# Performance work log

Measured on AMD Instinct MI355X. Metric: run time of the kernel, lower is better.

The kernel has to match this reference:

```python
import jax, jax.numpy as jnp
import numpy as np

N = 50000      # nodes
E = 600000     # edges
DIN = 128      # input_dim
H = 128        # hidden_dim
NH = 8         # heads
HD = H // NH   # head_dim = 16
OUT = 128      # output_dim
P = 20000      # pos/neg pair count
EPS = 1e-5


def setup_inputs() -> dict:
    key = jax.random.key(0)
    ks = jax.random.split(key, 20)
    s = 0.05
    inp = {
        "x": jax.random.normal(ks[0], (N, DIN), jnp.float32),
        "edge_index": jax.random.randint(ks[1], (2, E), 0, N),
        "drug_pos_ids": jax.random.randint(ks[2], (P,), 0, N),
        "target_pos_ids": jax.random.randint(ks[3], (P,), 0, N),
        "drug_neg_ids": jax.random.randint(ks[4], (P,), 0, N),
        "target_neg_ids": jax.random.randint(ks[5], (P,), 0, N),
        "adjacency_matrix": jnp.zeros((1,), jnp.float32),  # unused by forward
        # GCN weights stored [in, out]; biases [out]
        "gcn_w0": jax.random.normal(ks[6], (DIN, H), jnp.float32) * s,
        "gcn_b0": jnp.zeros((H,), jnp.float32),
        "gcn_w1": jax.random.normal(ks[7], (H, H), jnp.float32) * s,
        "gcn_b1": jnp.zeros((H,), jnp.float32),
        "gcn_w2": jax.random.normal(ks[8], (H, H), jnp.float32) * s,
        "gcn_b2": jnp.zeros((H,), jnp.float32),
        "wq": jax.random.normal(ks[9], (H, H), jnp.float32) * s,
        "wk": jax.random.normal(ks[10], (H, H), jnp.float32) * s,
        "wv": jax.random.normal(ks[11], (H, H), jnp.float32) * s,
        "ln_g": jnp.ones((H,), jnp.float32),   # shared LayerNorm (same instance reused)
        "ln_b": jnp.zeros((H,), jnp.float32),
        "out_w": jax.random.normal(ks[12], (H, OUT), jnp.float32) * s,
        "out_b": jnp.zeros((OUT,), jnp.float32),
    }
    return inp


def _layernorm(t, g, b):
    mu = t.mean(-1, keepdims=True)
    var = ((t - mu) ** 2).mean(-1, keepdims=True)
    return (t - mu) * jax.lax.rsqrt(var + EPS) * g + b


def reference(x, edge_index, drug_pos_ids, target_pos_ids, drug_neg_ids, target_neg_ids,
              adjacency_matrix, gcn_w0, gcn_b0, gcn_w1, gcn_b1, gcn_w2, gcn_b2,
              wq, wk, wv, ln_g, ln_b, out_w, out_b):
    num_nodes = x.shape[0]
    loop = jnp.arange(num_nodes)
    src = jnp.concatenate([edge_index[0], loop])  # add self-loops (PyG GCNConv default)
    dst = jnp.concatenate([edge_index[1], loop])
    deg = jax.ops.segment_sum(jnp.ones_like(dst, dtype=x.dtype), dst, num_segments=num_nodes)
    dinv = jnp.where(deg > 0, jax.lax.rsqrt(deg), 0.0)
    norm = dinv[src] * dinv[dst]  # [E+N]

    def gcn(h, W, b):
        hw = h @ W                                    # [N,H]
        msg = hw[src] * norm[:, None]                 # gather + scale  [E+N,H]
        return jax.ops.segment_sum(msg, dst, num_segments=num_nodes) + b

    cur = x
    embs = []
    for W, b in ((gcn_w0, gcn_b0), (gcn_w1, gcn_b1), (gcn_w2, gcn_b2)):
        new = jnp.maximum(gcn(cur, W, b), 0.0)
        new = _layernorm(new, ln_g, ln_b)
        # dropout is identity in eval mode
        cur = cur + new if cur.shape == new.shape else new
        embs.append(cur)
    emb = jnp.stack(embs, axis=0)  # [L,N,H]
    L = emb.shape[0]

    def split_heads(t):  # [L,N,H] -> [NH,N,L,HD]
        return t.reshape(L, num_nodes, NH, HD).transpose(2, 1, 0, 3)

    q = split_heads(emb @ wq)
    k = split_heads(emb @ wk)
    v = split_heads(emb @ wv)
    scores = jnp.einsum('hnld,hnmd->hnlm', q, k) / jnp.sqrt(jnp.float32(HD))
    attn = jax.nn.softmax(scores, axis=-1)  # dropout = identity in eval
    ctx = jnp.einsum('hnlm,hnmd->hnld', attn, v)          # [NH,N,L,HD]
    ctx = ctx.transpose(2, 1, 0, 3).reshape(L, num_nodes, H)

    z = _layernorm(ctx, ln_g, ln_b)
    z_last = z[-1] @ out_w + out_b  # [N,OUT]; z_D == z_T in original code
    return (z_last[drug_pos_ids], z_last[target_pos_ids],
            z_last[drug_neg_ids], z_last[target_neg_ids])
```

## Files before the change

kernel.cpp:

```cpp
#include <hip/hip_runtime.h>
#include <math.h>

using bf16x8 = __attribute__((ext_vector_type(8))) short;
using f32x4  = __attribute__((ext_vector_type(4))) float;

__device__ __forceinline__ unsigned short f2b(float f) {
  unsigned u = __float_as_uint(f);
  u += 0x7FFFu + ((u >> 16) & 1u);
  return (unsigned short)(u >> 16);
}
__device__ __forceinline__ float b2f(unsigned short h) {
  return __uint_as_float((unsigned)h << 16);
}
__device__ __forceinline__ float2 upk(unsigned u) {
  return make_float2(__uint_as_float(u << 16), __uint_as_float(u & 0xFFFF0000u));
}


__global__ void k_degree(const int* __restrict__ dst, int* __restrict__ degi, int E) {
  int e = blockIdx.x * blockDim.x + threadIdx.x;
  if (e < E) atomicAdd(&degi[dst[e]], 1);
}

__global__ void k_dinv(const int* __restrict__ degi, float* __restrict__ dinv, int n) {
  int i = blockIdx.x * blockDim.x + threadIdx.x;
  if (i < n) dinv[i] = rsqrtf((float)(degi[i] + 1));
}

__global__ __launch_bounds__(256)
void k_part(const int* __restrict__ deg, int* __restrict__ part, int n) {
  __shared__ int l[256];
  int tid = threadIdx.x, i = blockIdx.x * 256 + tid;
  l[tid] = (i < n) ? deg[i] : 0;
  __syncthreads();
  for (int s = 128; s; s >>= 1) { if (tid < s) l[tid] += l[tid + s]; __syncthreads(); }
  if (!tid) part[blockIdx.x] = l[0];
}

__global__ __launch_bounds__(1024)
void k_scanpart(int* __restrict__ part, int np, int* __restrict__ off_n) {
  __shared__ int l[1024];
  int tid = threadIdx.x;
  int v = (tid < np) ? part[tid] : 0;
  l[tid] = v;
  __syncthreads();
  for (int s = 1; s < 1024; s <<= 1) {
    int t = (tid >= s) ? l[tid - s] : 0;
    __syncthreads();
    l[tid] += t;
    __syncthreads();
  }
  if (tid < np) part[tid] = l[tid] - v;
  if (tid == np - 1) *off_n = l[tid];
}

__global__ __launch_bounds__(256)
void k_off(const int* __restrict__ deg, const int* __restrict__ part,
           int* __restrict__ off, int n) {
  __shared__ int l[256];
  int tid = threadIdx.x, i = blockIdx.x * 256 + tid;
  int v = (i < n) ? deg[i] : 0;
  l[tid] = v;
  __syncthreads();
  for (int s = 1; s < 256; s <<= 1) {
    int t = (tid >= s) ? l[tid - s] : 0;
    __syncthreads();
    l[tid] += t;
    __syncthreads();
  }
  if (i < n) off[i] = part[blockIdx.x] + l[tid] - v;
}

__global__ void k_scatter(const int* __restrict__ srcv, const int* __restrict__ dstv,
                          const float* __restrict__ dinv, const int* __restrict__ off,
                          int* __restrict__ cursor, int* __restrict__ csr_src,
                          float* __restrict__ csr_norm, int E) {
  int e = blockIdx.x * blockDim.x + threadIdx.x;
  if (e >= E) return;
  int d = dstv[e];
  int p = atomicAdd(&cursor[d], 1);
  int slot = off[d] + p;
  int s = srcv[e];
  csr_src[slot] = s;
  csr_norm[slot] = dinv[s] * dinv[d];
}


__global__ void k_cvtx(const float* __restrict__ x, unsigned short* __restrict__ xb,
                       long n4) {
  long t = (long)blockIdx.x * blockDim.x + threadIdx.x;
  if (t >= n4) return;
  float4 v = ((const float4*)x)[t];
  unsigned lo = (unsigned)f2b(v.x) | ((unsigned)f2b(v.y) << 16);
  unsigned hi = (unsigned)f2b(v.z) | ((unsigned)f2b(v.w) << 16);
  ((uint2*)xb)[t] = make_uint2(lo, hi);
}


__global__ __launch_bounds__(256)
void k_cvtw(const float* gw0, const float* gw1, const float* gw2,
            const float* wk, const float* wv, const float* wq, const float* ow,
            unsigned short* gwT0, unsigned short* gwT1, unsigned short* gwT2,
            unsigned short* wkvT, unsigned short* wqT, unsigned short* owT) {
  const float* src; unsigned short* dst;
  switch (blockIdx.y) {
    case 0: src = gw0; dst = gwT0; break;
    case 1: src = gw1; dst = gwT1; break;
    case 2: src = gw2; dst = gwT2; break;
    case 3: src = wk;  dst = wkvT; break;
    case 4: src = wv;  dst = wkvT + 128 * 128; break;
    case 5: src = wq;  dst = wqT; break;
    default: src = ow; dst = owT; break;
  }
  int t = blockIdx.x * 256 + threadIdx.x;
  int r = t >> 7, c = t & 127;
  dst[(long)c * 128 + r] = f2b(src[t]);
}


__global__ __launch_bounds__(128, 6)
void k_gcn_layer(const unsigned short* __restrict__ embp,
                 const int* __restrict__ off, const int* __restrict__ csr_src,
                 const float* __restrict__ csr_norm, const float* __restrict__ dinv,
                 const unsigned short* __restrict__ wT,
                 const float* __restrict__ bias,
                 const float* __restrict__ ln_g, const float* __restrict__ ln_b,
                 unsigned short* __restrict__ embo, int N) {
  __shared__ unsigned a_sw[16 * 64];
  __shared__ float lnsum[16][2], lnsq[16][2];

  int tid = threadIdx.x, lane = tid & 63, w = tid >> 6;
  int g = lane >> 4, c16 = lane & 15;
  long n0 = (long)blockIdx.x * 16;

  for (int t = 0; t < 8; ++t) {
    int row = w * 8 + t;
    long node = n0 + row;
    long nc = node < N ? node : N - 1;
    float dn = dinv[nc];
    int s0 = off[nc], s1 = off[nc + 1];
    float acc[8];
    {
      uint4 rs_ = *(const uint4*)&embp[nc * 128 + c16 * 8];
      float wgt = (g == 0) ? dn * dn : 0.f;
      float2 f;
      f = upk(rs_.x); acc[0] = f.x * wgt; acc[1] = f.y * wgt;
      f = upk(rs_.y); acc[2] = f.x * wgt; acc[3] = f.y * wgt;
      f = upk(rs_.z); acc[4] = f.x * wgt; acc[5] = f.y * wgt;
      f = upk(rs_.w); acc[6] = f.x * wgt; acc[7] = f.y * wgt;
    }
    for (int i = s0; i < s1; i += 16) {
      int id[4]; float nm[4];
#pragma unroll
      for (int u = 0; u < 4; ++u) {
        int j = i + u * 4 + g;
        int jj = j < s1 ? j : s1 - 1;
        id[u] = csr_src[jj];
        nm[u] = j < s1 ? csr_norm[jj] : 0.f;
      }
      uint4 rv[4];
#pragma unroll
      for (int u = 0; u < 4; ++u)
        rv[u] = *(const uint4*)&embp[(long)id[u] * 128 + c16 * 8];
#pragma unroll
      for (int u = 0; u < 4; ++u) {
        float2 f0 = upk(rv[u].x), f1 = upk(rv[u].y);
        float2 f2 = upk(rv[u].z), f3 = upk(rv[u].w);
        acc[0] += f0.x * nm[u]; acc[1] += f0.y * nm[u];
        acc[2] += f1.x * nm[u]; acc[3] += f1.y * nm[u];
        acc[4] += f2.x * nm[u]; acc[5] += f2.y * nm[u];
        acc[6] += f3.x * nm[u]; acc[7] += f3.y * nm[u];
      }
    }
#pragma unroll
    for (int k = 0; k < 8; ++k) {
      acc[k] += __shfl_xor(acc[k], 16);
      acc[k] += __shfl_xor(acc[k], 32);
    }
    if (g == 0) {
      unsigned* dst = (unsigned*)((char*)a_sw +
                      (row * 256 + ((c16 * 16) ^ ((row & 7) << 4))));
      dst[0] = (unsigned)f2b(acc[0]) | ((unsigned)f2b(acc[1]) << 16);
      dst[1] = (unsigned)f2b(acc[2]) | ((unsigned)f2b(acc[3]) << 16);
      dst[2] = (unsigned)f2b(acc[4]) | ((unsigned)f2b(acc[5]) << 16);
      dst[3] = (unsigned)f2b(acc[6]) | ((unsigned)f2b(acc[7]) << 16);
    }
  }
  __syncthreads();

  int lo = lane & 15, hi = lane >> 4;
  int cb0 = w * 64;
  f32x4 acc2[4] = {};
#pragma unroll
  for (int ks = 0; ks < 4; ++ks) {
    int k0 = ks * 32 + hi * 8;
    bf16x8 a = *(const bf16x8*)((char*)a_sw + lo * 256 + ((k0 * 2) ^ ((lo & 7) << 4)));
#pragma unroll
    for (int cf = 0; cf < 4; ++cf) {
      bf16x8 b = *(const bf16x8*)&wT[(long)(cb0 + cf * 16 + lo) * 128 + k0];
      acc2[cf] = __builtin_amdgcn_mfma_f32_16x16x32_bf16(a, b, acc2[cf], 0, 0, 0);
    }
  }

  float vreg[4][4];
#pragma unroll
  for (int j = 0; j < 4; ++j) {
    float s = 0.f, q = 0.f;
#pragma unroll
    for (int cf = 0; cf < 4; ++cf) {
      int col = cb0 + cf * 16 + lo;
      float v = fmaxf(acc2[cf][j] + bias[col], 0.f);
      vreg[cf][j] = v;
      s += v; q += v * v;
    }
#pragma unroll
    for (int m = 1; m < 16; m <<= 1) { s += __shfl_xor(s, m); q += __shfl_xor(q, m); }
    if (lo == 0) { lnsum[hi * 4 + j][w] = s; lnsq[hi * 4 + j][w] = q; }
  }
  __syncthreads();
#pragma unroll
  for (int j = 0; j < 4; ++j) {
    int row = hi * 4 + j;
    float sum = lnsum[row][0] + lnsum[row][1];
    float sq  = lnsq[row][0] + lnsq[row][1];
    float mu = sum * (1.f / 128.f);
    float var = sq * (1.f / 128.f) - mu * mu;
    float rs = rsqrtf(var + 1e-5f);
    long gr = n0 + row;
    if (gr < N) {
#pragma unroll
      for (int cf = 0; cf < 4; ++cf) {
        int col = cb0 + cf * 16 + lo;
        float z = (vreg[cf][j] - mu) * rs * ln_g[col] + ln_b[col]
                  + b2f(embp[gr * 128 + col]);
        embo[gr * 128 + col] = f2b(z);
      }
    }
  }
}


__global__ __launch_bounds__(256)
void k_attn_fused(const unsigned short* __restrict__ emb,
                  const unsigned short* __restrict__ wkvT,
                  const unsigned short* __restrict__ wqT,
                  const unsigned short* __restrict__ owT,
                  const float* __restrict__ ln_g, const float* __restrict__ ln_b,
                  const float* __restrict__ out_b,
                  unsigned short* __restrict__ zoutb, int N) {
  __shared__ unsigned short kvl[48 * 256];
  __shared__ unsigned short ql[16 * 128];
  __shared__ unsigned short zl[16 * 128];

  int tid = threadIdx.x, lane = tid & 63, w = tid >> 6;
  int lo = lane & 15, hi = lane >> 4;
  long n0 = (long)blockIdx.x * 16;
  long nr = n0 + lo; if (nr >= N) nr = N - 1;

  {
    int cb0 = w * 64;
    f32x4 acc[3][4] = {};
#pragma unroll
    for (int ks = 0; ks < 4; ++ks) {
      int k0 = ks * 32 + hi * 8;
      bf16x8 a[3];
#pragma unroll
      for (int l = 0; l < 3; ++l)
        a[l] = *(const bf16x8*)&emb[((long)l * N + nr) * 128 + k0];
#pragma unroll
      for (int cf = 0; cf < 4; ++cf) {
        bf16x8 b = *(const bf16x8*)&wkvT[(long)(cb0 + cf * 16 + lo) * 128 + k0];
#pragma unroll
        for (int l = 0; l < 3; ++l)
          acc[l][cf] = __builtin_amdgcn_mfma_f32_16x16x32_bf16(a[l], b, acc[l][cf], 0, 0, 0);
      }
    }
#pragma unroll
    for (int l = 0; l < 3; ++l)
#pragma unroll
      for (int cf = 0; cf < 4; ++cf)
#pragma unroll
        for (int j = 0; j < 4; ++j)
          kvl[(l * 16 + hi * 4 + j) * 256 + cb0 + cf * 16 + lo] = f2b(acc[l][cf][j]);
  }

  {
    int cq0 = w * 32;
    f32x4 aq[2] = {};
#pragma unroll
    for (int ks = 0; ks < 4; ++ks) {
      int k0 = ks * 32 + hi * 8;
      bf16x8 a = *(const bf16x8*)&emb[(2L * N + nr) * 128 + k0];
#pragma unroll
      for (int cf = 0; cf < 2; ++cf) {
        bf16x8 b = *(const bf16x8*)&wqT[(long)(cq0 + cf * 16 + lo) * 128 + k0];
        aq[cf] = __builtin_amdgcn_mfma_f32_16x16x32_bf16(a, b, aq[cf], 0, 0, 0);
      }
    }
#pragma unroll
    for (int cf = 0; cf < 2; ++cf)
#pragma unroll
      for (int j = 0; j < 4; ++j)
        ql[(hi * 4 + j) * 128 + cq0 + cf * 16 + lo] = f2b(aq[cf][j]);
  }
  __syncthreads();

  {
    const unsigned* kvu = (const unsigned*)kvl;
    const unsigned* qu  = (const unsigned*)ql;
    int c = lane * 2;
    float gx = ln_g[c], gy = ln_g[c + 1], bx = ln_b[c], by = ln_b[c + 1];
#pragma unroll
    for (int it = 0; it < 4; ++it) {
      int node = w * 4 + it;
      float2 q = upk(qu[node * 64 + lane]);
      float s[3], vx[3], vy[3];
#pragma unroll
      for (int m = 0; m < 3; ++m) {
        int row = m * 16 + node;
        float2 k = upk(kvu[row * 128 + lane]);
        float2 v = upk(kvu[row * 128 + 64 + lane]);
        float p = q.x * k.x + q.y * k.y;
        p += __shfl_xor(p, 1); p += __shfl_xor(p, 2); p += __shfl_xor(p, 4);
        s[m] = p * 0.25f;
        vx[m] = v.x; vy[m] = v.y;
      }
      float mx = fmaxf(s[0], fmaxf(s[1], s[2]));
      float e0 = __expf(s[0] - mx), e1 = __expf(s[1] - mx), e2 = __expf(s[2] - mx);
      float inv = 1.f / (e0 + e1 + e2);
      float cx = (e0 * vx[0] + e1 * vx[1] + e2 * vx[2]) * inv;
      float cy = (e0 * vy[0] + e1 * vy[1] + e2 * vy[2]) * inv;
      float sum = cx + cy, sq = cx * cx + cy * cy;
#pragma unroll
      for (int m = 1; m < 64; m <<= 1) { sum += __shfl_xor(sum, m); sq += __shfl_xor(sq, m); }
      float mu = sum * (1.f / 128.f);
      float var = sq * (1.f / 128.f) - mu * mu;
      float rs = rsqrtf(var + 1e-5f);
      unsigned pk = (unsigned)f2b((cx - mu) * rs * gx + bx) |
                    ((unsigned)f2b((cy - mu) * rs * gy + by) << 16);
      *(unsigned*)((char*)zl + node * 256 + ((lane * 4) ^ ((node & 7) << 4))) = pk;
    }
  }
  __syncthreads();

  {
    int co0 = w * 32;
    f32x4 ao[2] = {};
#pragma unroll
    for (int ks = 0; ks < 4; ++ks) {
      int k0 = ks * 32 + hi * 8;
      bf16x8 a = *(const bf16x8*)((const char*)zl + lo * 256 + (((k0 * 2) ^ ((lo & 7) << 4))));
#pragma unroll
      for (int cf = 0; cf < 2; ++cf) {
        bf16x8 b = *(const bf16x8*)&owT[(long)(co0 + cf * 16 + lo) * 128 + k0];
        ao[cf] = __builtin_amdgcn_mfma_f32_16x16x32_bf16(a, b, ao[cf], 0, 0, 0);
      }
    }
#pragma unroll
    for (int cf = 0; cf < 2; ++cf)
#pragma unroll
      for (int j = 0; j < 4; ++j) {
        long gn = n0 + hi * 4 + j;
        int col = co0 + cf * 16 + lo;
        if (gn < N) zoutb[gn * 128 + col] = f2b(ao[cf][j] + out_b[col]);
      }
  }
}


__global__ void k_gather4(const unsigned short* __restrict__ zoutb,
                          const int* __restrict__ ids0, const int* __restrict__ ids1,
                          const int* __restrict__ ids2, const int* __restrict__ ids3,
                          float* __restrict__ outp, int rows) {
  int t = blockIdx.x * blockDim.x + threadIdx.x;
  if (t >= rows * 16) return;
  int s = blockIdx.y;
  const int* ids = (s == 0) ? ids0 : (s == 1) ? ids1 : (s == 2) ? ids2 : ids3;
  int row = t >> 4, c8 = t & 15;
  long id = ids[row];
  uint4 v = *(const uint4*)&zoutb[id * 128 + c8 * 8];
  float2 f0 = upk(v.x), f1 = upk(v.y), f2_ = upk(v.z), f3 = upk(v.w);
  float4* dst = (float4*)&outp[(((long)s * rows + row) * 128) + c8 * 8];
  dst[0] = make_float4(f0.x, f0.y, f1.x, f1.y);
  dst[1] = make_float4(f2_.x, f2_.y, f3.x, f3.y);
}


extern "C" void kernel_launch(void* const* d_in, const int* in_sizes, int n_in,
                              void* d_out, int out_size, void* d_ws, size_t ws_size,
                              hipStream_t stream) {
  const float* x = (const float*)d_in[0];
  const int* ei = (const int*)d_in[1];
  const int* ids[4] = {(const int*)d_in[2], (const int*)d_in[3],
                       (const int*)d_in[4], (const int*)d_in[5]};
  const float* gw[3] = {(const float*)d_in[7], (const float*)d_in[9], (const float*)d_in[11]};
  const float* gb[3] = {(const float*)d_in[8], (const float*)d_in[10], (const float*)d_in[12]};
  const float* wq = (const float*)d_in[13];
  const float* wk = (const float*)d_in[14];
  const float* wv = (const float*)d_in[15];
  const float* ln_g = (const float*)d_in[16];
  const float* ln_b = (const float*)d_in[17];
  const float* out_w = (const float*)d_in[18];
  const float* out_b = (const float*)d_in[19];

  const int N = in_sizes[0] / 128;
  const int E = in_sizes[1] / 2;
  const int P = in_sizes[2];

  char* w = (char*)d_ws;
  size_t o = 0;
  auto take = [&](size_t bytes) -> void* {
    void* p = w + o;
    o = (o + bytes + 255) & ~(size_t)255;
    return p;
  };
  int*   degi    = (int*)take((size_t)N * 4);
  int*   off     = (int*)take((size_t)(N + 1) * 4);
  int*   cursor  = (int*)take((size_t)N * 4);
  int*   part    = (int*)take(1024 * 4);
  float* dinv    = (float*)take((size_t)N * 4);
  int*   csr_src = (int*)take((size_t)E * 4);
  float* csr_nrm = (float*)take((size_t)E * 4);
  unsigned short* gwT0 = (unsigned short*)take(128 * 128 * 2);
  unsigned short* gwT1 = (unsigned short*)take(128 * 128 * 2);
  unsigned short* gwT2 = (unsigned short*)take(128 * 128 * 2);
  unsigned short* wkvT = (unsigned short*)take(256 * 128 * 2);
  unsigned short* wqT  = (unsigned short*)take(128 * 128 * 2);
  unsigned short* owT  = (unsigned short*)take(128 * 128 * 2);
  unsigned short* xbf  = (unsigned short*)take((size_t)N * 128 * 2);
  unsigned short* emball = (unsigned short*)take((size_t)3 * N * 128 * 2);
  unsigned short* zoutb = (unsigned short*)take((size_t)N * 128 * 2);
  (void)ws_size; (void)n_in; (void)out_size;

  hipMemsetAsync(degi, 0, (size_t)N * 4, stream);
  hipMemsetAsync(cursor, 0, (size_t)N * 4, stream);

  int eb = (E + 255) / 256;
  int nb = (N + 255) / 256;
  k_degree<<<eb, 256, 0, stream>>>(ei + E, degi, E);
  k_dinv<<<nb, 256, 0, stream>>>(degi, dinv, N);
  k_part<<<nb, 256, 0, stream>>>(degi, part, N);
  k_scanpart<<<1, 1024, 0, stream>>>(part, nb, off + N);
  k_off<<<nb, 256, 0, stream>>>(degi, part, off, N);
  k_scatter<<<eb, 256, 0, stream>>>(ei, ei + E, dinv, off, cursor, csr_src, csr_nrm, E);
  k_cvtw<<<dim3(64, 7), 256, 0, stream>>>(gw[0], gw[1], gw[2], wk, wv, wq, out_w,
                                          gwT0, gwT1, gwT2, wkvT, wqT, owT);
  long n4 = (long)N * 32;
  k_cvtx<<<(int)((n4 + 255) / 256), 256, 0, stream>>>(x, xbf, n4);

  unsigned short* gwT[3] = {gwT0, gwT1, gwT2};
  int lgrid = (N + 15) / 16;
  const unsigned short* prev = xbf;
  for (int l = 0; l < 3; ++l) {
    unsigned short* outp = emball + (size_t)l * N * 128;
    k_gcn_layer<<<lgrid, 128, 0, stream>>>(prev, off, csr_src, csr_nrm, dinv,
                                           gwT[l], gb[l], ln_g, ln_b, outp, N);
    prev = outp;
  }

  k_attn_fused<<<(N + 15) / 16, 256, 0, stream>>>(emball, wkvT, wqT, owT,
                                                  ln_g, ln_b, out_b, zoutb, N);

  float* outf = (float*)d_out;
  int gb2 = (P * 16 + 255) / 256;
  k_gather4<<<dim3(gb2, 4), 256, 0, stream>>>(zoutb, ids[0], ids[1], ids[2], ids[3],
                                              outf, P);
}
```

Before: 305.5 us.

## Give each wave its own 16 nodes and keep attention in MFMA registers

The fused attention kernel now assigns each wave its own 16-node tile (64 nodes per block) instead of having four waves share 16 nodes. Q, K and V projections are computed per head directly in MFMA accumulator registers. Scores, softmax, context and LayerNorm are computed in registers with cross-lane shuffles, which removes the K/V/Q shared-memory staging and two block barriers. Only a small per-wave LDS tile is kept to feed the output projection. In exchange each wave does more MFMA work and holds more registers (launch_bounds 256,1), which may lower occupancy or cause spills, and the grid has a quarter as many blocks.

```diff
diff --git a/kernel.cpp b/kernel.cpp
--- a/kernel.cpp
+++ b/kernel.cpp
@@ -240,7 +240,7 @@
 }
 
 
-__global__ __launch_bounds__(256)
+__global__ __launch_bounds__(256, 1)
 void k_attn_fused(const unsigned short* __restrict__ emb,
                   const unsigned short* __restrict__ wkvT,
                   const unsigned short* __restrict__ wqT,
@@ -248,122 +248,122 @@
                   const float* __restrict__ ln_g, const float* __restrict__ ln_b,
                   const float* __restrict__ out_b,
                   unsigned short* __restrict__ zoutb, int N) {
-  __shared__ unsigned short kvl[48 * 256];
-  __shared__ unsigned short ql[16 * 128];
-  __shared__ unsigned short zl[16 * 128];
+  __shared__ unsigned short zl[4][16 * 128];
 
   int tid = threadIdx.x, lane = tid & 63, w = tid >> 6;
   int lo = lane & 15, hi = lane >> 4;
-  long n0 = (long)blockIdx.x * 16;
+  long n0 = (long)blockIdx.x * 64 + (long)w * 16;
   long nr = n0 + lo; if (nr >= N) nr = N - 1;
-
-  {
-    int cb0 = w * 64;
-    f32x4 acc[3][4] = {};
+  unsigned short* myz = zl[w];
+
+  bf16x8 a[3][4];
+#pragma unroll
+  for (int ks = 0; ks < 4; ++ks) {
+    int k0 = ks * 32 + hi * 8;
+#pragma unroll
+    for (int l = 0; l < 3; ++l)
+      a[l][ks] = *(const bf16x8*)&emb[((long)l * N + nr) * 128 + k0];
+  }
+
+  f32x4 qacc[8];
+#pragma unroll
+  for (int cf = 0; cf < 8; ++cf) {
+    f32x4 acc = {};
 #pragma unroll
     for (int ks = 0; ks < 4; ++ks) {
       int k0 = ks * 32 + hi * 8;
-      bf16x8 a[3];
-#pragma unroll
-      for (int l = 0; l < 3; ++l)
-        a[l] = *(const bf16x8*)&emb[((long)l * N + nr) * 128 + k0];
-#pragma unroll
-      for (int cf = 0; cf < 4; ++cf) {
-        bf16x8 b = *(const bf16x8*)&wkvT[(long)(cb0 + cf * 16 + lo) * 128 + k0];
-#pragma unroll
-        for (int l = 0; l < 3; ++l)
-          acc[l][cf] = __builtin_amdgcn_mfma_f32_16x16x32_bf16(a[l], b, acc[l][cf], 0, 0, 0);
-      }
-    }
-#pragma unroll
-    for (int l = 0; l < 3; ++l)
-#pragma unroll
-      for (int cf = 0; cf < 4; ++cf)
-#pragma unroll
-        for (int j = 0; j < 4; ++j)
-          kvl[(l * 16 + hi * 4 + j) * 256 + cb0 + cf * 16 + lo] = f2b(acc[l][cf][j]);
-  }
-
-  {
-    int cq0 = w * 32;
-    f32x4 aq[2] = {};
+      bf16x8 b = *(const bf16x8*)&wqT[(long)(cf * 16 + lo) * 128 + k0];
+      acc = __builtin_amdgcn_mfma_f32_16x16x32_bf16(a[2][ks], b, acc, 0, 0, 0);
+    }
+    qacc[cf] = acc;
+  }
+
+  f32x4 ctx[8];
+#pragma unroll
+  for (int h = 0; h < 8; ++h) {
+    f32x4 kacc[3] = {}, vacc[3] = {};
 #pragma unroll
     for (int ks = 0; ks < 4; ++ks) {
       int k0 = ks * 32 + hi * 8;
-      bf16x8 a = *(const bf16x8*)&emb[(2L * N + nr) * 128 + k0];
-#pragma unroll
-      for (int cf = 0; cf < 2; ++cf) {
-        bf16x8 b = *(const bf16x8*)&wqT[(long)(cq0 + cf * 16 + lo) * 128 + k0];
-        aq[cf] = __builtin_amdgcn_mfma_f32_16x16x32_bf16(a, b, aq[cf], 0, 0, 0);
+      bf16x8 bk = *(const bf16x8*)&wkvT[(long)(h * 16 + lo) * 128 + k0];
+      bf16x8 bv = *(const bf16x8*)&wkvT[(long)(128 + h * 16 + lo) * 128 + k0];
+#pragma unroll
+      for (int l = 0; l < 3; ++l) {
+        kacc[l] = __builtin_amdgcn_mfma_f32_16x16x32_bf16(a[l][ks], bk, kacc[l], 0, 0, 0);
+        vacc[l] = __builtin_amdgcn_mfma_f32_16x16x32_bf16(a[l][ks], bv, vacc[l], 0, 0, 0);
       }
     }
-#pragma unroll
-    for (int cf = 0; cf < 2; ++cf)
-#pragma unroll
-      for (int j = 0; j < 4; ++j)
-        ql[(hi * 4 + j) * 128 + cq0 + cf * 16 + lo] = f2b(aq[cf][j]);
-  }
-  __syncthreads();
-
-  {
-    const unsigned* kvu = (const unsigned*)kvl;
-    const unsigned* qu  = (const unsigned*)ql;
-    int c = lane * 2;
-    float gx = ln_g[c], gy = ln_g[c + 1], bx = ln_b[c], by = ln_b[c + 1];
-#pragma unroll
-    for (int it = 0; it < 4; ++it) {
-      int node = w * 4 + it;
-      float2 q = upk(qu[node * 64 + lane]);
-      float s[3], vx[3], vy[3];
-#pragma unroll
-      for (int m = 0; m < 3; ++m) {
-        int row = m * 16 + node;
-        float2 k = upk(kvu[row * 128 + lane]);
-        float2 v = upk(kvu[row * 128 + 64 + lane]);
-        float p = q.x * k.x + q.y * k.y;
-        p += __shfl_xor(p, 1); p += __shfl_xor(p, 2); p += __shfl_xor(p, 4);
-        s[m] = p * 0.25f;
-        vx[m] = v.x; vy[m] = v.y;
+    f32x4 p0 = qacc[h] * kacc[0];
+    f32x4 p1 = qacc[h] * kacc[1];
+    f32x4 p2 = qacc[h] * kacc[2];
+#pragma unroll
+    for (int m = 1; m < 16; m <<= 1) {
+#pragma unroll
+      for (int j = 0; j < 4; ++j) {
+        p0[j] += __shfl_xor(p0[j], m);
+        p1[j] += __shfl_xor(p1[j], m);
+        p2[j] += __shfl_xor(p2[j], m);
       }
-      float mx = fmaxf(s[0], fmaxf(s[1], s[2]));
-      float e0 = __expf(s[0] - mx), e1 = __expf(s[1] - mx), e2 = __expf(s[2] - mx);
-      float inv = 1.f / (e0 + e1 + e2);
-      float cx = (e0 * vx[0] + e1 * vx[1] + e2 * vx[2]) * inv;
-      float cy = (e0 * vy[0] + e1 * vy[1] + e2 * vy[2]) * inv;
-      float sum = cx + cy, sq = cx * cx + cy * cy;
-#pragma unroll
-      for (int m = 1; m < 64; m <<= 1) { sum += __shfl_xor(sum, m); sq += __shfl_xor(sq, m); }
-      float mu = sum * (1.f / 128.f);
-      float var = sq * (1.f / 128.f) - mu * mu;
-      float rs = rsqrtf(var + 1e-5f);
-      unsigned pk = (unsigned)f2b((cx - mu) * rs * gx + bx) |
-                    ((unsigned)f2b((cy - mu) * rs * gy + by) << 16);
-      *(unsigned*)((char*)zl + node * 256 + ((lane * 4) ^ ((node & 7) << 4))) = pk;
-    }
-  }
-  __syncthreads();
-
-  {
-    int co0 = w * 32;
-    f32x4 ao[2] = {};
+    }
+    f32x4 e0, e1, e2;
+#pragma unroll
+    for (int j = 0; j < 4; ++j) {
+      float x0 = p0[j] * 0.25f, x1 = p1[j] * 0.25f, x2 = p2[j] * 0.25f;
+      float mx = fmaxf(x0, fmaxf(x1, x2));
+      float a0 = __expf(x0 - mx), a1 = __expf(x1 - mx), a2 = __expf(x2 - mx);
+      float inv = 1.f / (a0 + a1 + a2);
+      e0[j] = a0 * inv; e1[j] = a1 * inv; e2[j] = a2 * inv;
+    }
+    ctx[h] = e0 * vacc[0] + e1 * vacc[1] + e2 * vacc[2];
+  }
+
+  f32x4 sum = {}, sq = {};
+#pragma unroll
+  for (int h = 0; h < 8; ++h) { sum += ctx[h]; sq += ctx[h] * ctx[h]; }
+#pragma unroll
+  for (int m = 1; m < 16; m <<= 1) {
+#pragma unroll
+    for (int j = 0; j < 4; ++j) {
+      sum[j] += __shfl_xor(sum[j], m);
+      sq[j]  += __shfl_xor(sq[j], m);
+    }
+  }
+#pragma unroll
+  for (int j = 0; j < 4; ++j) {
+    float mu = sum[j] * (1.f / 128.f);
+    float var = sq[j] * (1.f / 128.f) - mu * mu;
+    float rs = rsqrtf(var + 1e-5f);
+    int node = hi * 4 + j;
+#pragma unroll
+    for (int h = 0; h < 8; ++h) {
+      int ch = h * 16 + lo;
+      float z = (ctx[h][j] - mu) * rs * ln_g[ch] + ln_b[ch];
+      *(unsigned short*)((char*)myz + node * 256 + ((ch * 2) ^ ((node & 7) << 4))) = f2b(z);
+    }
+  }
+
+  bf16x8 az[4];
+#pragma unroll
+  for (int ks = 0; ks < 4; ++ks) {
+    int k0 = ks * 32 + hi * 8;
+    az[ks] = *(const bf16x8*)((const char*)myz + lo * 256 + ((k0 * 2) ^ ((lo & 7) << 4)));
+  }
+#pragma unroll
+  for (int cf = 0; cf < 8; ++cf) {
+    f32x4 acc = {};
 #pragma unroll
     for (int ks = 0; ks < 4; ++ks) {
       int k0 = ks * 32 + hi * 8;
-      bf16x8 a = *(const bf16x8*)((const char*)zl + lo * 256 + (((k0 * 2) ^ ((lo & 7) << 4))));
-#pragma unroll
-      for (int cf = 0; cf < 2; ++cf) {
-        bf16x8 b = *(const bf16x8*)&owT[(long)(co0 + cf * 16 + lo) * 128 + k0];
-        ao[cf] = __builtin_amdgcn_mfma_f32_16x16x32_bf16(a, b, ao[cf], 0, 0, 0);
-      }
-    }
-#pragma unroll
-    for (int cf = 0; cf < 2; ++cf)
-#pragma unroll
-      for (int j = 0; j < 4; ++j) {
-        long gn = n0 + hi * 4 + j;
-        int col = co0 + cf * 16 + lo;
-        if (gn < N) zoutb[gn * 128 + col] = f2b(ao[cf][j] + out_b[col]);
-      }
+      bf16x8 b = *(const bf16x8*)&owT[(long)(cf * 16 + lo) * 128 + k0];
+      acc = __builtin_amdgcn_mfma_f32_16x16x32_bf16(az[ks], b, acc, 0, 0, 0);
+    }
+    int col = cf * 16 + lo;
+    float ob = out_b[col];
+#pragma unroll
+    for (int j = 0; j < 4; ++j) {
+      long gn = n0 + hi * 4 + j;
+      if (gn < N) zoutb[gn * 128 + col] = f2b(acc[j] + ob);
+    }
   }
 }
 
@@ -458,7 +458,7 @@
     prev = outp;
   }
 
-  k_attn_fused<<<(N + 15) / 16, 256, 0, stream>>>(emball, wkvT, wqT, owT,
+  k_attn_fused<<<(N + 63) / 64, 256, 0, stream>>>(emball, wkvT, wqT, owT,
                                                   ln_g, ln_b, out_b, zoutb, N);
 
   float* outf = (float*)d_out;
```

Measured after the change: 302.0 us. About the same (-1.1%).
